# Optimization experiments

Measured on AMD Instinct MI355X. Metric: run time of the kernel, lower is better.

## Reference

```python
import jax, jax.numpy as jnp
import numpy as np

N, E, D, H, HID = 50000, 400000, 64, 8, 1024
NEG_SLOPE = 0.2
BN_EPS = 1e-5


def setup_inputs() -> dict:
    key = jax.random.key(0)
    ks = jax.random.split(key, 10)
    s = 0.05
    return {
        "x": jax.random.normal(ks[0], (N, D), jnp.float32),
        "src": jax.random.randint(ks[1], (E,), 0, N, jnp.int32),
        "dst": jax.random.randint(ks[2], (E,), 0, N, jnp.int32),
        "fc_w": jax.random.normal(ks[3], (H * D, D), jnp.float32) * s,
        "attn_l": jax.random.normal(ks[4], (H, D), jnp.float32) * s,
        "attn_r": jax.random.normal(ks[5], (H, D), jnp.float32) * s,
        "gat_bias": jnp.zeros((H * D,), jnp.float32),
        "bn1_gamma": jnp.ones((H * D,), jnp.float32),
        "bn1_beta": jnp.zeros((H * D,), jnp.float32),
        "w1": jax.random.normal(ks[6], (HID, H * D), jnp.float32) * s,
        "b1": jnp.zeros((HID,), jnp.float32),
        "w2": jax.random.normal(ks[7], (D, HID), jnp.float32) * s,
        "b2": jnp.zeros((D,), jnp.float32),
        "bn2_gamma": jnp.ones((D,), jnp.float32),
        "bn2_beta": jnp.zeros((D,), jnp.float32),
    }


def _batchnorm(h, gamma, beta):
    # training-mode BatchNorm1d: batch statistics over node axis
    mu = h.mean(axis=0)
    var = h.var(axis=0)
    return gamma * (h - mu) * jax.lax.rsqrt(var + BN_EPS) + beta


def reference(x, src, dst, fc_w, attn_l, attn_r, gat_bias,
              bn1_gamma, bn1_beta, w1, b1, w2, b2, bn2_gamma, bn2_beta):
    n = x.shape[0]
    nh, dh = attn_l.shape
    # --- GATConv ---
    feat = (x @ fc_w.T).reshape(n, nh, dh)                 # [N,H,Dh]
    el = jnp.einsum("nhd,hd->nh", feat, attn_l)            # [N,H]
    er = jnp.einsum("nhd,hd->nh", feat, attn_r)            # [N,H]
    e = jax.nn.leaky_relu(el[src] + er[dst], NEG_SLOPE)    # [E,H]
    # edge softmax grouped by destination node (numerically stable)
    emax = jax.ops.segment_max(e, dst, num_segments=n)
    emax = jnp.where(jnp.isfinite(emax), emax, 0.0)        # nodes w/ no in-edges
    ez = jnp.exp(e - emax[dst])
    denom = jax.ops.segment_sum(ez, dst, num_segments=n)
    alpha = ez / denom[dst]                                # [E,H]
    msg = alpha[:, :, None] * feat[src]                    # [E,H,Dh]
    rst = jax.ops.segment_sum(msg, dst, num_segments=n)    # [N,H,Dh]
    rst = rst + gat_bias.reshape(nh, dh)
    h = rst.reshape(n, nh * dh)                            # flatten(1)
    # --- feed forward: BN -> Linear -> ReLU -> Linear -> BN ---
    h = _batchnorm(h, bn1_gamma, bn1_beta)
    h = jax.nn.relu(h @ w1.T + b1)
    h = h @ w2.T + b2
    h = _batchnorm(h, bn2_gamma, bn2_beta)
    return h
```

## Files before the change

### kernel.cpp

```cpp
#include <hip/hip_runtime.h>

#define NEG_SLOPE 0.2f
#define BN_EPS 1e-5f

typedef __bf16 bf16x8 __attribute__((ext_vector_type(8)));
typedef float  f32x4  __attribute__((ext_vector_type(4)));
typedef unsigned short ushort8_t __attribute__((ext_vector_type(8)));

__device__ __forceinline__ unsigned short f2bf(float f) {
    unsigned int u = __float_as_uint(f);
    unsigned int r = u + 0x7FFFu + ((u >> 16) & 1u);
    return (unsigned short)(r >> 16);
}
__device__ __forceinline__ float bf2f(unsigned short u) {
    return __uint_as_float(((unsigned int)u) << 16);
}
__device__ __forceinline__ void gload16(const void* g, void* l) {
    __builtin_amdgcn_global_load_lds(
        (const __attribute__((address_space(1))) unsigned int*)g,
        (__attribute__((address_space(3))) unsigned int*)l, 16, 0, 0);
}

__global__ __launch_bounds__(256)
void gemm1_mfma(const unsigned short* __restrict__ Ax, const unsigned short* __restrict__ Bw,
                unsigned short* __restrict__ C,
                const float* __restrict__ attn_l, const float* __restrict__ attn_r,
                float* __restrict__ el, float* __restrict__ er, int M)
{
    __shared__ alignas(16) char Asm[128 * 64 * 2];
    __shared__ alignas(16) char Bsm[128 * 64 * 2];
    const int tid = threadIdx.x, lane = tid & 63, wave = tid >> 6;
    const int wr = wave >> 1, wc = wave & 1;
    const int bm = blockIdx.x * 128, bn = blockIdx.y * 128;
    const int lr = lane >> 3, lk = ((lane & 7) ^ (lane >> 3)) * 8;

    #pragma unroll
    for (int it = 0; it < 4; ++it) {
        int seg = wave * 4 + it;
        gload16(Ax + (size_t)(bm + seg * 8 + lr) * 64 + lk, Asm + seg * 1024);
        gload16(Bw + (size_t)(bn + seg * 8 + lr) * 64 + lk, Bsm + seg * 1024);
    }
    __syncthreads();

    f32x4 acc[4][4] = {};
    #pragma unroll
    for (int kk = 0; kk < 2; ++kk) {
        int kg = kk * 4 + (lane >> 4);
        bf16x8 a[4], b[4];
        #pragma unroll
        for (int i = 0; i < 4; ++i) {
            int row = wr * 64 + i * 16 + (lane & 15);
            a[i] = *(const bf16x8*)(Asm + row * 128 + ((kg ^ (row & 7)) << 4));
        }
        #pragma unroll
        for (int j = 0; j < 4; ++j) {
            int row = wc * 64 + j * 16 + (lane & 15);
            b[j] = *(const bf16x8*)(Bsm + row * 128 + ((kg ^ (row & 7)) << 4));
        }
        #pragma unroll
        for (int i = 0; i < 4; ++i)
            #pragma unroll
            for (int j = 0; j < 4; ++j)
                acc[i][j] = __builtin_amdgcn_mfma_f32_16x16x32_bf16(a[i], b[j], acc[i][j], 0, 0, 0);
    }

    #pragma unroll
    for (int j = 0; j < 4; ++j) {
        int gn = bn + wc * 64 + j * 16 + (lane & 15);
        #pragma unroll
        for (int i = 0; i < 4; ++i)
            #pragma unroll
            for (int r = 0; r < 4; ++r) {
                int gm = bm + wr * 64 + i * 16 + (lane >> 4) * 4 + r;
                if (gm < M) C[(size_t)gm * 512 + gn] = f2bf(acc[i][j][r]);
            }
    }

    const int head = (bn >> 6) + wc;
    float al[4], ar[4];
    #pragma unroll
    for (int j = 0; j < 4; ++j) {
        int c = j * 16 + (lane & 15);
        al[j] = attn_l[head * 64 + c];
        ar[j] = attn_r[head * 64 + c];
    }
    #pragma unroll
    for (int i = 0; i < 4; ++i)
        #pragma unroll
        for (int r = 0; r < 4; ++r) {
            int gm = bm + wr * 64 + i * 16 + (lane >> 4) * 4 + r;
            float sl = 0.f, sr = 0.f;
            #pragma unroll
            for (int j = 0; j < 4; ++j) {
                sl = fmaf(acc[i][j][r], al[j], sl);
                sr = fmaf(acc[i][j][r], ar[j], sr);
            }
            sl += __shfl_xor(sl, 1); sr += __shfl_xor(sr, 1);
            sl += __shfl_xor(sl, 2); sr += __shfl_xor(sr, 2);
            sl += __shfl_xor(sl, 4); sr += __shfl_xor(sr, 4);
            sl += __shfl_xor(sl, 8); sr += __shfl_xor(sr, 8);
            if ((lane & 15) == 0 && gm < M) {
                el[gm * 8 + head] = sl;
                er[gm * 8 + head] = sr;
            }
        }
}

__global__ __launch_bounds__(256)
void gemm2p(const unsigned short* __restrict__ A,
            const unsigned short* __restrict__ B,
            const unsigned short* __restrict__ W2,
            const float* __restrict__ b1p,
            unsigned short* __restrict__ P,
            int M)
{
    __shared__ alignas(16) char smem[49152];
    char* Abuf0 = smem;
    char* Abuf1 = smem + 16384;
    char* Bbuf  = smem + 32768;
    char* TR   = smem;
    char* Wbuf = smem + 32768;
    char* PK   = smem + 32768;

    const int tid = threadIdx.x, lane = tid & 63, wave = tid >> 6;
    const int wr = wave >> 1, wc = wave & 1;
    const int lr = lane >> 3, lk = ((lane & 7) ^ lr) * 8;

    int bid = blockIdx.x;
    int wgid = (bid & 7) * 391 + (bid >> 3);
    const int bm = (wgid >> 3) * 128;
    const int t  = wgid & 7;
    const int bn = t * 128;

    #pragma unroll
    for (int it = 0; it < 4; ++it) {
        int seg = wave * 4 + it;
        gload16(A + (size_t)(bm + seg * 8 + lr) * 512 + lk, Abuf0 + seg * 1024);
    }

    f32x4 acc[4][4] = {};
    #pragma unroll
    for (int ks = 0; ks < 8; ++ks) {
        const int k0 = ks * 64;
        #pragma unroll
        for (int it = 0; it < 4; ++it) {
            int seg = wave * 4 + it;
            gload16(B + (size_t)(bn + seg * 8 + lr) * 512 + k0 + lk, Bbuf + seg * 1024);
        }
        if (ks < 7) {
            char* An = (ks & 1) ? Abuf0 : Abuf1;
            #pragma unroll
            for (int it = 0; it < 4; ++it) {
                int seg = wave * 4 + it;
                gload16(A + (size_t)(bm + seg * 8 + lr) * 512 + (k0 + 64) + lk, An + seg * 1024);
            }
            asm volatile("s_waitcnt vmcnt(4)" ::: "memory");
        } else {
            asm volatile("s_waitcnt vmcnt(0)" ::: "memory");
        }
        __builtin_amdgcn_s_barrier();
        __builtin_amdgcn_sched_barrier(0);
        const char* Ac = (ks & 1) ? Abuf1 : Abuf0;
        #pragma unroll
        for (int kk = 0; kk < 2; ++kk) {
            int kg = kk * 4 + (lane >> 4);
            bf16x8 a[4], b[4];
            #pragma unroll
            for (int i = 0; i < 4; ++i) {
                int row = wr * 64 + i * 16 + (lane & 15);
                a[i] = *(const bf16x8*)(Ac + row * 128 + ((kg ^ (row & 7)) << 4));
            }
            #pragma unroll
            for (int j = 0; j < 4; ++j) {
                int row = wc * 64 + j * 16 + (lane & 15);
                b[j] = *(const bf16x8*)(Bbuf + row * 128 + ((kg ^ (row & 7)) << 4));
            }
            #pragma unroll
            for (int i = 0; i < 4; ++i)
                #pragma unroll
                for (int j = 0; j < 4; ++j)
                    acc[i][j] = __builtin_amdgcn_mfma_f32_16x16x32_bf16(a[i], b[j], acc[i][j], 0, 0, 0);
        }
        __builtin_amdgcn_sched_barrier(0);
        __builtin_amdgcn_s_barrier();
        __builtin_amdgcn_sched_barrier(0);
    }

    #pragma unroll
    for (int j = 0; j < 4; ++j) {
        int c = wc * 64 + j * 16 + (lane & 15);
        float bs = b1p[bn + c];
        #pragma unroll
        for (int i = 0; i < 4; ++i)
            #pragma unroll
            for (int r = 0; r < 4; ++r) {
                int rw = wr * 64 + i * 16 + (lane >> 4) * 4 + r;
                float v = fmaxf(acc[i][j][r] + bs, 0.f);
                *(unsigned short*)(TR + rw * 256 + (((c >> 3) ^ (rw & 7)) << 4) + (c & 7) * 2) = f2bf(v);
            }
    }
    #pragma unroll
    for (int it = 0; it < 4; ++it) {
        int oc = wave * 16 + it * 4 + (lane >> 4);
        int g = lane & 15;
        gload16(W2 + (size_t)oc * 1024 + bn + ((g ^ (oc & 7))) * 8, Wbuf + (wave * 4 + it) * 1024);
    }
    __syncthreads();

    f32x4 pacc[2][4] = {};
    #pragma unroll
    for (int ks = 0; ks < 4; ++ks) {
        int kg2 = ks * 4 + (lane >> 4);
        #pragma unroll
        for (int i = 0; i < 2; ++i) {
            int arow = wave * 32 + i * 16 + (lane & 15);
            bf16x8 av = *(const bf16x8*)(TR + arow * 256 + ((kg2 ^ (arow & 7)) << 4));
            #pragma unroll
            for (int j = 0; j < 4; ++j) {
                int oc = j * 16 + (lane & 15);
                bf16x8 bv = *(const bf16x8*)(Wbuf + oc * 256 + ((kg2 ^ (oc & 7)) << 4));
                pacc[i][j] = __builtin_amdgcn_mfma_f32_16x16x32_bf16(av, bv, pacc[i][j], 0, 0, 0);
            }
        }
    }
    __syncthreads();

    #pragma unroll
    for (int i = 0; i < 2; ++i)
        #pragma unroll
        for (int j = 0; j < 4; ++j)
            #pragma unroll
            for (int r = 0; r < 4; ++r) {
                int row = wave * 32 + i * 16 + (lane >> 4) * 4 + r;
                int col = j * 16 + (lane & 15);
                *(unsigned short*)(PK + row * 128 + col * 2) = f2bf(pacc[i][j][r]);
            }
    __syncthreads();
    unsigned short* Pt = P + (size_t)t * M * 64;
    #pragma unroll
    for (int it = 0; it < 4; ++it) {
        int u = it * 256 + tid;
        int row = u >> 3, g8 = u & 7;
        int gm = bm + row;
        if (gm < M) {
            uint4 v = *(const uint4*)(PK + row * 128 + g8 * 16);
            *(uint4*)(Pt + (size_t)gm * 64 + g8 * 8) = v;
        }
    }
}

__global__ __launch_bounds__(256)
void reduce_bn2(const unsigned short* __restrict__ P, const float* __restrict__ b2,
                float* __restrict__ out, int M, float* __restrict__ sums2)
{
    __shared__ float ls[256], lq[256];
    int c = threadIdx.x & 63, g = threadIdx.x >> 6;
    const size_t S = (size_t)M * 64;
    float bias = b2[c];
    float s = 0.f, q = 0.f;
    for (int r = blockIdx.x * 4 + g; r < M; r += gridDim.x * 4) {
        size_t idx = (size_t)r * 64 + c;
        float v = bias;
        #pragma unroll
        for (int t = 0; t < 8; ++t) v += bf2f(P[t * S + idx]);
        out[idx] = v;
        s += v; q += v * v;
    }
    ls[threadIdx.x] = s; lq[threadIdx.x] = q;
    __syncthreads();
    if (g == 0) {
        s = ls[c] + ls[64 + c] + ls[128 + c] + ls[192 + c];
        q = lq[c] + lq[64 + c] + lq[128 + c] + lq[192 + c];
        atomicAdd(&sums2[c], s);
        atomicAdd(&sums2[64 + c], q);
    }
}

__global__ void hist_kernel(const int* __restrict__ dst, int* __restrict__ counts, int E) {
    int i = blockIdx.x * 256 + threadIdx.x;
    if (i < E) atomicAdd(&counts[dst[i]], 1);
}
__global__ void scan1(const int* __restrict__ counts, int* __restrict__ incl,
                      int* __restrict__ bsum, int N) {
    __shared__ int sm[256];
    int i = blockIdx.x * 256 + threadIdx.x;
    int v = (i < N) ? counts[i] : 0;
    sm[threadIdx.x] = v;
    __syncthreads();
    #pragma unroll
    for (int d = 1; d < 256; d <<= 1) {
        int t = (threadIdx.x >= d) ? sm[threadIdx.x - d] : 0;
        __syncthreads();
        sm[threadIdx.x] += t;
        __syncthreads();
    }
    if (i < N) incl[i] = sm[threadIdx.x];
    if (threadIdx.x == 255) bsum[blockIdx.x] = sm[255];
}
__global__ void scan2(int* __restrict__ bsum, int nb) {
    __shared__ int sm[256];
    int v = (threadIdx.x < nb) ? bsum[threadIdx.x] : 0;
    sm[threadIdx.x] = v;
    __syncthreads();
    #pragma unroll
    for (int d = 1; d < 256; d <<= 1) {
        int t = (threadIdx.x >= d) ? sm[threadIdx.x - d] : 0;
        __syncthreads();
        sm[threadIdx.x] += t;
        __syncthreads();
    }
    if (threadIdx.x < nb) bsum[threadIdx.x] = sm[threadIdx.x] - v;
}
__global__ void scan3(const int* __restrict__ incl, const int* __restrict__ bsum,
                      int* __restrict__ row_ptr, int N) {
    int i = blockIdx.x * 256 + threadIdx.x;
    if (i < N) row_ptr[i + 1] = incl[i] + bsum[blockIdx.x];
    if (i == 0) row_ptr[0] = 0;
}
__global__ void scatter_edges(const int* __restrict__ src, const int* __restrict__ dst,
                              int* __restrict__ cursor, int* __restrict__ esrc, int E) {
    int e = blockIdx.x * 256 + threadIdx.x;
    if (e < E) {
        int p = atomicAdd(&cursor[dst[e]], 1);
        esrc[p] = src[e];
    }
}

__global__ __launch_bounds__(256)
void gat_aggregate(const int* __restrict__ row_ptr, const int* __restrict__ esrc,
                   const float* __restrict__ el, const float* __restrict__ er,
                   const unsigned short* __restrict__ feat, const float* __restrict__ gat_bias,
                   unsigned short* __restrict__ hout, int N)
{
    int node = blockIdx.x * 4 + (threadIdx.x >> 6);
    if (node >= N) return;
    const int lane = threadIdx.x & 63;
    const int h = lane >> 3, j = lane & 7;
    const int beg = row_ptr[node], end = row_ptr[node + 1];
    const float er_n = er[node * 8 + h];

    float m = -INFINITY;
    for (int k = beg + j; k < end; k += 8) {
        int s = esrc[k];
        float v = el[s * 8 + h] + er_n;
        v = (v > 0.f) ? v : NEG_SLOPE * v;
        m = fmaxf(m, v);
    }
    m = fmaxf(m, __shfl_xor(m, 1));
    m = fmaxf(m, __shfl_xor(m, 2));
    m = fmaxf(m, __shfl_xor(m, 4));

    float denom = 0.f;
    float a[8] = {};
    for (int k = beg; k < end; ++k) {
        int s = esrc[k];
        float v = el[s * 8 + h] + er_n;
        v = (v > 0.f) ? v : NEG_SLOPE * v;
        float z = __expf(v - m);
        denom += z;
        ushort8_t fv = *(const ushort8_t*)(feat + (size_t)s * 512 + lane * 8);
        #pragma unroll
        for (int t = 0; t < 8; ++t) a[t] = fmaf(z, bf2f(fv[t]), a[t]);
    }
    float inv = (end > beg) ? 1.f / denom : 0.f;
    ushort8_t o;
    #pragma unroll
    for (int t = 0; t < 8; ++t) o[t] = f2bf(fmaf(a[t], inv, gat_bias[lane * 8 + t]));
    *(ushort8_t*)(hout + (size_t)node * 512 + lane * 8) = o;
}

__global__ __launch_bounds__(256)
void bn_stats512bf(const unsigned short* __restrict__ X, int M, float* __restrict__ sums)
{
    __shared__ float red[4][512];
    int cg = threadIdx.x & 63, rg = threadIdx.x >> 6;
    float s[8] = {}, q[8] = {};
    for (int r = blockIdx.x * 4 + rg; r < M; r += gridDim.x * 4) {
        ushort8_t v = *(const ushort8_t*)(X + (size_t)r * 512 + cg * 8);
        #pragma unroll
        for (int t = 0; t < 8; ++t) { float f = bf2f(v[t]); s[t] += f; q[t] += f * f; }
    }
    #pragma unroll
    for (int t = 0; t < 8; ++t) red[rg][cg * 8 + t] = s[t];
    __syncthreads();
    if (rg == 0)
        #pragma unroll
        for (int t = 0; t < 8; ++t) {
            int c = cg * 8 + t;
            atomicAdd(&sums[c], red[0][c] + red[1][c] + red[2][c] + red[3][c]);
        }
    __syncthreads();
    #pragma unroll
    for (int t = 0; t < 8; ++t) red[rg][cg * 8 + t] = q[t];
    __syncthreads();
    if (rg == 0)
        #pragma unroll
        for (int t = 0; t < 8; ++t) {
            int c = cg * 8 + t;
            atomicAdd(&sums[512 + c], red[0][c] + red[1][c] + red[2][c] + red[3][c]);
        }
}

__global__ __launch_bounds__(256)
void fold_w1(const float* __restrict__ w1, const float* __restrict__ ab1,
             const float* __restrict__ b1, unsigned short* __restrict__ w1p,
             float* __restrict__ b1p)
{
    int n = blockIdx.x * 4 + (threadIdx.x >> 6);
    int lane = threadIdx.x & 63;
    const float* wrow = w1 + (size_t)n * 512 + lane * 8;
    float p = 0.f;
    ushort8_t o;
    #pragma unroll
    for (int t = 0; t < 8; ++t) {
        float w = wrow[t];
        o[t] = f2bf(w * ab1[lane * 8 + t]);
        p = fmaf(w, ab1[512 + lane * 8 + t], p);
    }
    *(ushort8_t*)(w1p + (size_t)n * 512 + lane * 8) = o;
    #pragma unroll
    for (int d = 1; d < 64; d <<= 1) p += __shfl_xor(p, d);
    if (lane == 0) b1p[n] = b1[n] + p;
}

__global__ void cvt_f32_bf16(const float* __restrict__ s, unsigned short* __restrict__ d, int n) {
    int i = blockIdx.x * 256 + threadIdx.x;
    if (i < n) d[i] = f2bf(s[i]);
}

__global__ void bn_finalize(const float* __restrict__ sums, const float* __restrict__ gamma,
                            const float* __restrict__ beta, float* __restrict__ ab,
                            int C, float invM)
{
    int c = blockIdx.x * blockDim.x + threadIdx.x;
    if (c >= C) return;
    float mu = sums[c] * invM;
    float var = sums[C + c] * invM - mu * mu;
    float a = gamma[c] * rsqrtf(var + BN_EPS);
    ab[c] = a;
    ab[C + c] = beta[c] - a * mu;
}

__global__ __launch_bounds__(256)
void bn_apply64(float* __restrict__ X, const float* __restrict__ ab, int total)
{
    int idx = blockIdx.x * 256 + threadIdx.x;
    if (idx >= total) return;
    int c = idx & 63;
    X[idx] = fmaf(ab[c], X[idx], ab[64 + c]);
}

extern "C" void kernel_launch(void* const* d_in, const int* in_sizes, int n_in,
                              void* d_out, int out_size, void* d_ws, size_t ws_size,
                              hipStream_t stream)
{
    const float* x         = (const float*)d_in[0];
    const int*   src       = (const int*)d_in[1];
    const int*   dst       = (const int*)d_in[2];
    const float* fc_w      = (const float*)d_in[3];
    const float* attn_l    = (const float*)d_in[4];
    const float* attn_r    = (const float*)d_in[5];
    const float* gat_bias  = (const float*)d_in[6];
    const float* bn1_gamma = (const float*)d_in[7];
    const float* bn1_beta  = (const float*)d_in[8];
    const float* w1        = (const float*)d_in[9];
    const float* b1        = (const float*)d_in[10];
    const float* w2        = (const float*)d_in[11];
    const float* b2        = (const float*)d_in[12];
    const float* bn2_gamma = (const float*)d_in[13];
    const float* bn2_beta  = (const float*)d_in[14];
    float* out = (float*)d_out;

    const int D = 64, HD = 512, HID = 1024;
    const int N = in_sizes[0] / D;
    const int E = in_sizes[1];
    const int NH = N * 8;
    const int NB = (N + 255) / 256;
    const int Mpad = ((N + 127) / 128) * 128 + 128;

    size_t off = 0;
    auto alloc = [&](size_t bytes) -> void* {
        void* p = (char*)d_ws + off;
        off += (bytes + 255) & ~(size_t)255;
        return p;
    };
    void* regionA = alloc((size_t)N * HD * 2);
    unsigned short* feat = (unsigned short*)regionA;
    unsigned short* P    = (unsigned short*)regionA;
    unsigned short* hbf  = (unsigned short*)alloc((size_t)Mpad * HD * 2);
    unsigned short* xbf  = (unsigned short*)alloc((size_t)Mpad * D * 2);
    unsigned short* fcwbf = (unsigned short*)alloc((size_t)HD * D * 2);
    unsigned short* w1p  = (unsigned short*)alloc((size_t)HID * HD * 2);
    unsigned short* w2bf = (unsigned short*)alloc((size_t)D * HID * 2);
    float* b1p   = (float*)alloc(HID * 4);
    float* el    = (float*)alloc((size_t)NH * 4);
    float* er    = (float*)alloc((size_t)NH * 4);
    int* counts  = (int*)alloc((size_t)N * 4);
    int* incl    = (int*)alloc((size_t)N * 4);
    int* row_ptr = (int*)alloc((size_t)(N + 1) * 4);
    int* cursor  = (int*)alloc((size_t)N * 4);
    int* bsum    = (int*)alloc(256 * 4);
    int* esrc    = (int*)alloc((size_t)E * 4);
    float* sums1 = (float*)alloc(2 * 512 * 4);
    float* ab1   = (float*)alloc(2 * 512 * 4);
    float* sums2 = (float*)alloc(2 * 64 * 4);
    float* ab2   = (float*)alloc(2 * 64 * 4);
    (void)ws_size; (void)n_in; (void)out_size;

    hipMemsetAsync(counts, 0, (size_t)N * 4, stream);
    hist_kernel<<<(E + 255) / 256, 256, 0, stream>>>(dst, counts, E);
    scan1<<<NB, 256, 0, stream>>>(counts, incl, bsum, N);
    scan2<<<1, 256, 0, stream>>>(bsum, NB);
    scan3<<<NB, 256, 0, stream>>>(incl, bsum, row_ptr, N);
    hipMemcpyAsync(cursor, row_ptr, (size_t)N * 4, hipMemcpyDeviceToDevice, stream);
    scatter_edges<<<(E + 255) / 256, 256, 0, stream>>>(src, dst, cursor, esrc, E);

    cvt_f32_bf16<<<(N * D + 255) / 256, 256, 0, stream>>>(x, xbf, N * D);
    cvt_f32_bf16<<<(HD * D + 255) / 256, 256, 0, stream>>>(fc_w, fcwbf, HD * D);
    cvt_f32_bf16<<<(D * HID + 255) / 256, 256, 0, stream>>>(w2, w2bf, D * HID);

    {
        dim3 grid((N + 127) / 128, HD / 128);
        gemm1_mfma<<<grid, 256, 0, stream>>>(xbf, fcwbf, feat, attn_l, attn_r, el, er, N);
    }

    gat_aggregate<<<(N + 3) / 4, 256, 0, stream>>>(row_ptr, esrc, el, er, feat,
                                                   gat_bias, hbf, N);

    hipMemsetAsync(sums1, 0, 2 * 512 * 4, stream);
    bn_stats512bf<<<256, 256, 0, stream>>>(hbf, N, sums1);
    bn_finalize<<<2, 256, 0, stream>>>(sums1, bn1_gamma, bn1_beta, ab1, HD, 1.f / N);
    fold_w1<<<HID / 4, 256, 0, stream>>>(w1, ab1, b1, w1p, b1p);

    {
        int nwg = ((N + 127) / 128) * 8;
        gemm2p<<<nwg, 256, 0, stream>>>(hbf, w1p, w2bf, b1p, P, N);
    }

    hipMemsetAsync(sums2, 0, 2 * 64 * 4, stream);
    reduce_bn2<<<256, 256, 0, stream>>>(P, b2, out, N, sums2);
    bn_finalize<<<1, 64, 0, stream>>>(sums2, bn2_gamma, bn2_beta, ab2, D, 1.f / N);
    bn_apply64<<<((N * D) + 255) / 256, 256, 0, stream>>>(out, ab2, N * D);
}
```

Baseline: 347.6 us.

## Aggregate raw inputs before projection and fuse BN1 statistics into head GEMM

```diff
diff --git a/kernel.cpp b/kernel.cpp
--- a/kernel.cpp
+++ b/kernel.cpp
@@ -21,89 +21,246 @@
         (__attribute__((address_space(3))) unsigned int*)l, 16, 0, 0);
 }
 
-__global__ __launch_bounds__(256)
-void gemm1_mfma(const unsigned short* __restrict__ Ax, const unsigned short* __restrict__ Bw,
-                unsigned short* __restrict__ C,
-                const float* __restrict__ attn_l, const float* __restrict__ attn_r,
-                float* __restrict__ el, float* __restrict__ er, int M)
+__global__ void build_proj(const float* __restrict__ fc_w, const float* __restrict__ attn_l,
+                           const float* __restrict__ attn_r, float* __restrict__ proj)
+{
+    int t = threadIdx.x;
+    int h = t >> 6, k = t & 63;
+    float al = 0.f, ar = 0.f;
+    for (int d = 0; d < 64; ++d) {
+        float w = fc_w[(size_t)(h * 64 + d) * 64 + k];
+        al = fmaf(attn_l[h * 64 + d], w, al);
+        ar = fmaf(attn_r[h * 64 + d], w, ar);
+    }
+    proj[t] = al;
+    proj[512 + t] = ar;
+}
+
+__global__ __launch_bounds__(256)
+void elr_kernel(const float* __restrict__ x, const float* __restrict__ proj,
+                float* __restrict__ el, float* __restrict__ er, int NH)
+{
+    int idx = blockIdx.x * 256 + threadIdx.x;
+    if (idx >= NH) return;
+    int h = idx & 7, n = idx >> 3;
+    const float4* f  = (const float4*)(x + (size_t)n * 64);
+    const float4* pl = (const float4*)(proj + h * 64);
+    const float4* pr = (const float4*)(proj + 512 + h * 64);
+    float sl = 0.f, sr = 0.f;
+    #pragma unroll
+    for (int i = 0; i < 16; ++i) {
+        float4 fv = f[i], lv = pl[i], rv = pr[i];
+        sl += fv.x * lv.x + fv.y * lv.y + fv.z * lv.z + fv.w * lv.w;
+        sr += fv.x * rv.x + fv.y * rv.y + fv.z * rv.z + fv.w * rv.w;
+    }
+    el[idx] = sl;
+    er[idx] = sr;
+}
+
+__global__ void hist_kernel(const int* __restrict__ dst, int* __restrict__ counts, int E) {
+    int i = blockIdx.x * 256 + threadIdx.x;
+    if (i < E) atomicAdd(&counts[dst[i]], 1);
+}
+__global__ void scan1(const int* __restrict__ counts, int* __restrict__ incl,
+                      int* __restrict__ bsum, int N) {
+    __shared__ int sm[256];
+    int i = blockIdx.x * 256 + threadIdx.x;
+    int v = (i < N) ? counts[i] : 0;
+    sm[threadIdx.x] = v;
+    __syncthreads();
+    #pragma unroll
+    for (int d = 1; d < 256; d <<= 1) {
+        int t = (threadIdx.x >= d) ? sm[threadIdx.x - d] : 0;
+        __syncthreads();
+        sm[threadIdx.x] += t;
+        __syncthreads();
+    }
+    if (i < N) incl[i] = sm[threadIdx.x];
+    if (threadIdx.x == 255) bsum[blockIdx.x] = sm[255];
+}
+__global__ void scan2(int* __restrict__ bsum, int nb) {
+    __shared__ int sm[256];
+    int v = (threadIdx.x < nb) ? bsum[threadIdx.x] : 0;
+    sm[threadIdx.x] = v;
+    __syncthreads();
+    #pragma unroll
+    for (int d = 1; d < 256; d <<= 1) {
+        int t = (threadIdx.x >= d) ? sm[threadIdx.x - d] : 0;
+        __syncthreads();
+        sm[threadIdx.x] += t;
+        __syncthreads();
+    }
+    if (threadIdx.x < nb) bsum[threadIdx.x] = sm[threadIdx.x] - v;
+}
+__global__ void scan3(const int* __restrict__ incl, const int* __restrict__ bsum,
+                      int* __restrict__ row_ptr, int N) {
+    int i = blockIdx.x * 256 + threadIdx.x;
+    if (i < N) row_ptr[i + 1] = incl[i] + bsum[blockIdx.x];
+    if (i == 0) row_ptr[0] = 0;
+}
+__global__ void scatter_edges(const int* __restrict__ src, const int* __restrict__ dst,
+                              int* __restrict__ cursor, int* __restrict__ esrc, int E) {
+    int e = blockIdx.x * 256 + threadIdx.x;
+    if (e < E) {
+        int p = atomicAdd(&cursor[dst[e]], 1);
+        esrc[p] = src[e];
+    }
+}
+
+__global__ __launch_bounds__(256)
+void gat_aggregate(const int* __restrict__ row_ptr, const int* __restrict__ esrc,
+                   const float* __restrict__ el, const float* __restrict__ er,
+                   const unsigned short* __restrict__ xb, unsigned short* __restrict__ xagg,
+                   int N)
+{
+    int node = blockIdx.x * 4 + (threadIdx.x >> 6);
+    if (node >= N) return;
+    const int lane = threadIdx.x & 63;
+    const int h = lane >> 3, j = lane & 7;
+    const int beg = row_ptr[node], end = row_ptr[node + 1];
+    const float er_n = er[node * 8 + h];
+
+    float m = -INFINITY;
+    for (int k = beg + j; k < end; k += 8) {
+        int s = esrc[k];
+        float v = el[s * 8 + h] + er_n;
+        v = (v > 0.f) ? v : NEG_SLOPE * v;
+        m = fmaxf(m, v);
+    }
+    m = fmaxf(m, __shfl_xor(m, 1));
+    m = fmaxf(m, __shfl_xor(m, 2));
+    m = fmaxf(m, __shfl_xor(m, 4));
+
+    float denom = 0.f;
+    float a[8] = {};
+    for (int k = beg; k < end; ++k) {
+        int s = esrc[k];
+        float v = el[s * 8 + h] + er_n;
+        v = (v > 0.f) ? v : NEG_SLOPE * v;
+        float z = __expf(v - m);
+        denom += z;
+        ushort8_t fv = *(const ushort8_t*)(xb + (size_t)s * 64 + j * 8);
+        #pragma unroll
+        for (int t = 0; t < 8; ++t) a[t] = fmaf(z, bf2f(fv[t]), a[t]);
+    }
+    float inv = (end > beg) ? 1.f / denom : 0.f;
+    ushort8_t o;
+    #pragma unroll
+    for (int t = 0; t < 8; ++t) o[t] = f2bf(a[t] * inv);
+    *(ushort8_t*)(xagg + (size_t)node * 512 + lane * 8) = o;
+}
+
+__global__ __launch_bounds__(256)
+void head_transform(const unsigned short* __restrict__ Xa,
+                    const unsigned short* __restrict__ Fw,
+                    const float* __restrict__ gat_bias,
+                    unsigned short* __restrict__ H,
+                    float* __restrict__ sums1,
+                    int M)
 {
     __shared__ alignas(16) char Asm[128 * 64 * 2];
-    __shared__ alignas(16) char Bsm[128 * 64 * 2];
+    __shared__ alignas(16) char Bsm[64 * 64 * 2];
+    __shared__ float reds[4][64], redq[4][64];
     const int tid = threadIdx.x, lane = tid & 63, wave = tid >> 6;
-    const int wr = wave >> 1, wc = wave & 1;
-    const int bm = blockIdx.x * 128, bn = blockIdx.y * 128;
-    const int lr = lane >> 3, lk = ((lane & 7) ^ (lane >> 3)) * 8;
+    const int bm = blockIdx.x * 128;
+    const int head = blockIdx.y;
+    const int lr = lane >> 3, lk = ((lane & 7) ^ lr) * 8;
 
     #pragma unroll
     for (int it = 0; it < 4; ++it) {
         int seg = wave * 4 + it;
-        gload16(Ax + (size_t)(bm + seg * 8 + lr) * 64 + lk, Asm + seg * 1024);
-        gload16(Bw + (size_t)(bn + seg * 8 + lr) * 64 + lk, Bsm + seg * 1024);
-    }
-    __syncthreads();
-
-    f32x4 acc[4][4] = {};
+        gload16(Xa + (size_t)(bm + seg * 8 + lr) * 512 + head * 64 + lk, Asm + seg * 1024);
+    }
+    #pragma unroll
+    for (int it = 0; it < 2; ++it) {
+        int seg = wave * 2 + it;
+        gload16(Fw + (size_t)(head * 64 + seg * 8 + lr) * 64 + lk, Bsm + seg * 1024);
+    }
+    __syncthreads();
+
+    f32x4 acc[2][4] = {};
     #pragma unroll
     for (int kk = 0; kk < 2; ++kk) {
         int kg = kk * 4 + (lane >> 4);
-        bf16x8 a[4], b[4];
-        #pragma unroll
-        for (int i = 0; i < 4; ++i) {
-            int row = wr * 64 + i * 16 + (lane & 15);
+        bf16x8 a[2], b[4];
+        #pragma unroll
+        for (int i = 0; i < 2; ++i) {
+            int row = wave * 32 + i * 16 + (lane & 15);
             a[i] = *(const bf16x8*)(Asm + row * 128 + ((kg ^ (row & 7)) << 4));
         }
         #pragma unroll
         for (int j = 0; j < 4; ++j) {
-            int row = wc * 64 + j * 16 + (lane & 15);
+            int row = j * 16 + (lane & 15);
             b[j] = *(const bf16x8*)(Bsm + row * 128 + ((kg ^ (row & 7)) << 4));
         }
         #pragma unroll
-        for (int i = 0; i < 4; ++i)
+        for (int i = 0; i < 2; ++i)
             #pragma unroll
             for (int j = 0; j < 4; ++j)
                 acc[i][j] = __builtin_amdgcn_mfma_f32_16x16x32_bf16(a[i], b[j], acc[i][j], 0, 0, 0);
     }
 
+    float s4[4] = {}, q4[4] = {};
     #pragma unroll
     for (int j = 0; j < 4; ++j) {
-        int gn = bn + wc * 64 + j * 16 + (lane & 15);
-        #pragma unroll
-        for (int i = 0; i < 4; ++i)
+        int col = j * 16 + (lane & 15);
+        float bias = gat_bias[head * 64 + col];
+        #pragma unroll
+        for (int i = 0; i < 2; ++i)
             #pragma unroll
             for (int r = 0; r < 4; ++r) {
-                int gm = bm + wr * 64 + i * 16 + (lane >> 4) * 4 + r;
-                if (gm < M) C[(size_t)gm * 512 + gn] = f2bf(acc[i][j][r]);
-            }
-    }
-
-    const int head = (bn >> 6) + wc;
-    float al[4], ar[4];
+                int gm = bm + wave * 32 + i * 16 + (lane >> 4) * 4 + r;
+                if (gm < M) {
+                    unsigned short hb = f2bf(acc[i][j][r] + bias);
+                    H[(size_t)gm * 512 + head * 64 + col] = hb;
+                    float vq = bf2f(hb);
+                    s4[j] += vq; q4[j] += vq * vq;
+                }
+            }
+    }
     #pragma unroll
     for (int j = 0; j < 4; ++j) {
-        int c = j * 16 + (lane & 15);
-        al[j] = attn_l[head * 64 + c];
-        ar[j] = attn_r[head * 64 + c];
-    }
-    #pragma unroll
-    for (int i = 0; i < 4; ++i)
-        #pragma unroll
-        for (int r = 0; r < 4; ++r) {
-            int gm = bm + wr * 64 + i * 16 + (lane >> 4) * 4 + r;
-            float sl = 0.f, sr = 0.f;
-            #pragma unroll
-            for (int j = 0; j < 4; ++j) {
-                sl = fmaf(acc[i][j][r], al[j], sl);
-                sr = fmaf(acc[i][j][r], ar[j], sr);
-            }
-            sl += __shfl_xor(sl, 1); sr += __shfl_xor(sr, 1);
-            sl += __shfl_xor(sl, 2); sr += __shfl_xor(sr, 2);
-            sl += __shfl_xor(sl, 4); sr += __shfl_xor(sr, 4);
-            sl += __shfl_xor(sl, 8); sr += __shfl_xor(sr, 8);
-            if ((lane & 15) == 0 && gm < M) {
-                el[gm * 8 + head] = sl;
-                er[gm * 8 + head] = sr;
-            }
-        }
+        s4[j] += __shfl_xor(s4[j], 16); q4[j] += __shfl_xor(q4[j], 16);
+        s4[j] += __shfl_xor(s4[j], 32); q4[j] += __shfl_xor(q4[j], 32);
+    }
+    if (lane < 16) {
+        #pragma unroll
+        for (int j = 0; j < 4; ++j) {
+            reds[wave][j * 16 + lane] = s4[j];
+            redq[wave][j * 16 + lane] = q4[j];
+        }
+    }
+    __syncthreads();
+    if (wave == 0 && lane < 16) {
+        #pragma unroll
+        for (int j = 0; j < 4; ++j) {
+            int c = j * 16 + lane;
+            atomicAdd(&sums1[head * 64 + c], reds[0][c] + reds[1][c] + reds[2][c] + reds[3][c]);
+            atomicAdd(&sums1[512 + head * 64 + c], redq[0][c] + redq[1][c] + redq[2][c] + redq[3][c]);
+        }
+    }
+}
+
+__global__ __launch_bounds__(256)
+void fold_w1(const float* __restrict__ w1, const float* __restrict__ ab1,
+             const float* __restrict__ b1, unsigned short* __restrict__ w1p,
+             float* __restrict__ b1p)
+{
+    int n = blockIdx.x * 4 + (threadIdx.x >> 6);
+    int lane = threadIdx.x & 63;
+    const float* wrow = w1 + (size_t)n * 512 + lane * 8;
+    float p = 0.f;
+    ushort8_t o;
+    #pragma unroll
+    for (int t = 0; t < 8; ++t) {
+        float w = wrow[t];
+        o[t] = f2bf(w * ab1[lane * 8 + t]);
+        p = fmaf(w, ab1[512 + lane * 8 + t], p);
+    }
+    *(ushort8_t*)(w1p + (size_t)n * 512 + lane * 8) = o;
+    #pragma unroll
+    for (int d = 1; d < 64; d <<= 1) p += __shfl_xor(p, d);
+    if (lane == 0) b1p[n] = b1[n] + p;
 }
 
 __global__ __launch_bounds__(256)
@@ -274,153 +431,6 @@
         atomicAdd(&sums2[c], s);
         atomicAdd(&sums2[64 + c], q);
     }
-}
-
-__global__ void hist_kernel(const int* __restrict__ dst, int* __restrict__ counts, int E) {
-    int i = blockIdx.x * 256 + threadIdx.x;
-    if (i < E) atomicAdd(&counts[dst[i]], 1);
-}
-__global__ void scan1(const int* __restrict__ counts, int* __restrict__ incl,
-                      int* __restrict__ bsum, int N) {
-    __shared__ int sm[256];
-    int i = blockIdx.x * 256 + threadIdx.x;
-    int v = (i < N) ? counts[i] : 0;
-    sm[threadIdx.x] = v;
-    __syncthreads();
-    #pragma unroll
-    for (int d = 1; d < 256; d <<= 1) {
-        int t = (threadIdx.x >= d) ? sm[threadIdx.x - d] : 0;
-        __syncthreads();
-        sm[threadIdx.x] += t;
-        __syncthreads();
-    }
-    if (i < N) incl[i] = sm[threadIdx.x];
-    if (threadIdx.x == 255) bsum[blockIdx.x] = sm[255];
-}
-__global__ void scan2(int* __restrict__ bsum, int nb) {
-    __shared__ int sm[256];
-    int v = (threadIdx.x < nb) ? bsum[threadIdx.x] : 0;
-    sm[threadIdx.x] = v;
-    __syncthreads();
-    #pragma unroll
-    for (int d = 1; d < 256; d <<= 1) {
-        int t = (threadIdx.x >= d) ? sm[threadIdx.x - d] : 0;
-        __syncthreads();
-        sm[threadIdx.x] += t;
-        __syncthreads();
-    }
-    if (threadIdx.x < nb) bsum[threadIdx.x] = sm[threadIdx.x] - v;
-}
-__global__ void scan3(const int* __restrict__ incl, const int* __restrict__ bsum,
-                      int* __restrict__ row_ptr, int N) {
-    int i = blockIdx.x * 256 + threadIdx.x;
-    if (i < N) row_ptr[i + 1] = incl[i] + bsum[blockIdx.x];
-    if (i == 0) row_ptr[0] = 0;
-}
-__global__ void scatter_edges(const int* __restrict__ src, const int* __restrict__ dst,
-                              int* __restrict__ cursor, int* __restrict__ esrc, int E) {
-    int e = blockIdx.x * 256 + threadIdx.x;
-    if (e < E) {
-        int p = atomicAdd(&cursor[dst[e]], 1);
-        esrc[p] = src[e];
-    }
-}
-
-__global__ __launch_bounds__(256)
-void gat_aggregate(const int* __restrict__ row_ptr, const int* __restrict__ esrc,
-                   const float* __restrict__ el, const float* __restrict__ er,
-                   const unsigned short* __restrict__ feat, const float* __restrict__ gat_bias,
-                   unsigned short* __restrict__ hout, int N)
-{
-    int node = blockIdx.x * 4 + (threadIdx.x >> 6);
-    if (node >= N) return;
-    const int lane = threadIdx.x & 63;
-    const int h = lane >> 3, j = lane & 7;
-    const int beg = row_ptr[node], end = row_ptr[node + 1];
-    const float er_n = er[node * 8 + h];
-
-    float m = -INFINITY;
-    for (int k = beg + j; k < end; k += 8) {
-        int s = esrc[k];
-        float v = el[s * 8 + h] + er_n;
-        v = (v > 0.f) ? v : NEG_SLOPE * v;
-        m = fmaxf(m, v);
-    }
-    m = fmaxf(m, __shfl_xor(m, 1));
-    m = fmaxf(m, __shfl_xor(m, 2));
-    m = fmaxf(m, __shfl_xor(m, 4));
-
-    float denom = 0.f;
-    float a[8] = {};
-    for (int k = beg; k < end; ++k) {
-        int s = esrc[k];
-        float v = el[s * 8 + h] + er_n;
-        v = (v > 0.f) ? v : NEG_SLOPE * v;
-        float z = __expf(v - m);
-        denom += z;
-        ushort8_t fv = *(const ushort8_t*)(feat + (size_t)s * 512 + lane * 8);
-        #pragma unroll
-        for (int t = 0; t < 8; ++t) a[t] = fmaf(z, bf2f(fv[t]), a[t]);
-    }
-    float inv = (end > beg) ? 1.f / denom : 0.f;
-    ushort8_t o;
-    #pragma unroll
-    for (int t = 0; t < 8; ++t) o[t] = f2bf(fmaf(a[t], inv, gat_bias[lane * 8 + t]));
-    *(ushort8_t*)(hout + (size_t)node * 512 + lane * 8) = o;
-}
-
-__global__ __launch_bounds__(256)
-void bn_stats512bf(const unsigned short* __restrict__ X, int M, float* __restrict__ sums)
-{
-    __shared__ float red[4][512];
-    int cg = threadIdx.x & 63, rg = threadIdx.x >> 6;
-    float s[8] = {}, q[8] = {};
-    for (int r = blockIdx.x * 4 + rg; r < M; r += gridDim.x * 4) {
-        ushort8_t v = *(const ushort8_t*)(X + (size_t)r * 512 + cg * 8);
-        #pragma unroll
-        for (int t = 0; t < 8; ++t) { float f = bf2f(v[t]); s[t] += f; q[t] += f * f; }
-    }
-    #pragma unroll
-    for (int t = 0; t < 8; ++t) red[rg][cg * 8 + t] = s[t];
-    __syncthreads();
-    if (rg == 0)
-        #pragma unroll
-        for (int t = 0; t < 8; ++t) {
-            int c = cg * 8 + t;
-            atomicAdd(&sums[c], red[0][c] + red[1][c] + red[2][c] + red[3][c]);
-        }
-    __syncthreads();
-    #pragma unroll
-    for (int t = 0; t < 8; ++t) red[rg][cg * 8 + t] = q[t];
-    __syncthreads();
-    if (rg == 0)
-        #pragma unroll
-        for (int t = 0; t < 8; ++t) {
-            int c = cg * 8 + t;
-            atomicAdd(&sums[512 + c], red[0][c] + red[1][c] + red[2][c] + red[3][c]);
-        }
-}
-
-__global__ __launch_bounds__(256)
-void fold_w1(const float* __restrict__ w1, const float* __restrict__ ab1,
-             const float* __restrict__ b1, unsigned short* __restrict__ w1p,
-             float* __restrict__ b1p)
-{
-    int n = blockIdx.x * 4 + (threadIdx.x >> 6);
-    int lane = threadIdx.x & 63;
-    const float* wrow = w1 + (size_t)n * 512 + lane * 8;
-    float p = 0.f;
-    ushort8_t o;
-    #pragma unroll
-    for (int t = 0; t < 8; ++t) {
-        float w = wrow[t];
-        o[t] = f2bf(w * ab1[lane * 8 + t]);
-        p = fmaf(w, ab1[512 + lane * 8 + t], p);
-    }
-    *(ushort8_t*)(w1p + (size_t)n * 512 + lane * 8) = o;
-    #pragma unroll
-    for (int d = 1; d < 64; d <<= 1) p += __shfl_xor(p, d);
-    if (lane == 0) b1p[n] = b1[n] + p;
 }
 
 __global__ void cvt_f32_bf16(const float* __restrict__ s, unsigned short* __restrict__ d, int n) {
@@ -484,15 +494,16 @@
         off += (bytes + 255) & ~(size_t)255;
         return p;
     };
-    void* regionA = alloc((size_t)N * HD * 2);
-    unsigned short* feat = (unsigned short*)regionA;
+    void* regionA = alloc((size_t)Mpad * HD * 2);
+    unsigned short* xagg = (unsigned short*)regionA;
     unsigned short* P    = (unsigned short*)regionA;
     unsigned short* hbf  = (unsigned short*)alloc((size_t)Mpad * HD * 2);
-    unsigned short* xbf  = (unsigned short*)alloc((size_t)Mpad * D * 2);
+    unsigned short* xbf  = (unsigned short*)alloc((size_t)N * D * 2);
     unsigned short* fcwbf = (unsigned short*)alloc((size_t)HD * D * 2);
     unsigned short* w1p  = (unsigned short*)alloc((size_t)HID * HD * 2);
     unsigned short* w2bf = (unsigned short*)alloc((size_t)D * HID * 2);
     float* b1p   = (float*)alloc(HID * 4);
+    float* proj  = (float*)alloc(2 * 512 * 4);
     float* el    = (float*)alloc((size_t)NH * 4);
     float* er    = (float*)alloc((size_t)NH * 4);
     int* counts  = (int*)alloc((size_t)N * 4);
@@ -518,17 +529,16 @@
     cvt_f32_bf16<<<(N * D + 255) / 256, 256, 0, stream>>>(x, xbf, N * D);
     cvt_f32_bf16<<<(HD * D + 255) / 256, 256, 0, stream>>>(fc_w, fcwbf, HD * D);
     cvt_f32_bf16<<<(D * HID + 255) / 256, 256, 0, stream>>>(w2, w2bf, D * HID);
-
+    build_proj<<<1, 512, 0, stream>>>(fc_w, attn_l, attn_r, proj);
+    elr_kernel<<<(NH + 255) / 256, 256, 0, stream>>>(x, proj, el, er, NH);
+
+    gat_aggregate<<<(N + 3) / 4, 256, 0, stream>>>(row_ptr, esrc, el, er, xbf, xagg, N);
+
+    hipMemsetAsync(sums1, 0, 2 * 512 * 4, stream);
     {
-        dim3 grid((N + 127) / 128, HD / 128);
-        gemm1_mfma<<<grid, 256, 0, stream>>>(xbf, fcwbf, feat, attn_l, attn_r, el, er, N);
-    }
-
-    gat_aggregate<<<(N + 3) / 4, 256, 0, stream>>>(row_ptr, esrc, el, er, feat,
-                                                   gat_bias, hbf, N);
-
-    hipMemsetAsync(sums1, 0, 2 * 512 * 4, stream);
-    bn_stats512bf<<<256, 256, 0, stream>>>(hbf, N, sums1);
+        dim3 grid((N + 127) / 128, 8);
+        head_transform<<<grid, 256, 0, stream>>>(xagg, fcwbf, gat_bias, hbf, sums1, N);
+    }
     bn_finalize<<<2, 256, 0, stream>>>(sums1, bn1_gamma, bn1_beta, ab1, HD, 1.f / N);
     fold_w1<<<HID / 4, 256, 0, stream>>>(w1, ab1, b1, w1p, b1p);
 
```

Measured after the change: 309.5 us. 1.12x faster.
